# Performance work log

Measured on AMD Instinct MI355X. Metric: run time of the kernel, lower is better.

## Reference

```python
import jax, jax.numpy as jnp
import numpy as np

C = 128          # hidden_channels
N = 100000       # num nodes
E = 500000       # num edges
BN_EPS = 1e-5    # BatchNorm eps (training mode: batch statistics)


def _bn_relu(x, g, b):
    # BatchNorm1d (training mode, biased variance) followed by ReLU
    mu = x.mean(axis=0)
    var = x.var(axis=0)
    return jax.nn.relu(g * (x - mu) * jax.lax.rsqrt(var + BN_EPS) + b)


def setup_inputs() -> dict:
    key = jax.random.key(0)
    ks = jax.random.split(key, 10)
    f = lambda k, s: jax.random.normal(k, s, dtype=jnp.float32) * 0.05
    return {
        "node_rep": f(ks[0], (N, C)),
        "edge_rep": f(ks[1], (E, C)),
        "endpoints": jax.random.randint(ks[2], (2, E), 0, N, dtype=jnp.int64)
            if jax.config.jax_enable_x64 else jax.random.randint(ks[2], (2, E), 0, N, dtype=jnp.int32),
        # lvl_mlp_1: Linear(2C -> C, no bias) + BN(C)
        "W_lvl1": f(ks[3], (2 * C, C)),
        "g_lvl1": jnp.ones((C,), jnp.float32), "b_lvl1": jnp.zeros((C,), jnp.float32),
        # lvl_mlp_2: Linear(C->2C) + BN(2C) + ReLU + Linear(2C->C) + BN(C) + ReLU
        "W_n1": f(ks[4], (C, 2 * C)),
        "g_n1": jnp.ones((2 * C,), jnp.float32), "b_n1": jnp.zeros((2 * C,), jnp.float32),
        "W_n2": f(ks[5], (2 * C, C)),
        "g_n2": jnp.ones((C,), jnp.float32), "b_n2": jnp.zeros((C,), jnp.float32),
        # lift_mlp: Linear(C->2C) + BN(2C) + ReLU + Linear(2C->C) + BN(C) + ReLU
        "W_e1": f(ks[6], (C, 2 * C)),
        "g_e1": jnp.ones((2 * C,), jnp.float32), "b_e1": jnp.zeros((2 * C,), jnp.float32),
        "W_e2": f(ks[7], (2 * C, C)),
        "g_e2": jnp.ones((C,), jnp.float32), "b_e2": jnp.zeros((C,), jnp.float32),
        "eps1": jnp.zeros((), jnp.float32),
        "eps2": jnp.zeros((), jnp.float32),
    }


def reference(node_rep, edge_rep, endpoints,
              W_lvl1, g_lvl1, b_lvl1,
              W_n1, g_n1, b_n1, W_n2, g_n2, b_n2,
              W_e1, g_e1, b_e1, W_e2, g_e2, b_e2,
              eps1, eps2):
    s, t = endpoints[0], endpoints[1]
    # transfer0_0 node->edge: each edge sums its two endpoint node features
    lift_aggr = node_rep[s] + node_rep[t]                       # [E, C]
    h = _bn_relu(jnp.concatenate([lift_aggr, edge_rep], -1) @ W_lvl1,
                 g_lvl1, b_lvl1)                                # [E, C]
    # reverse transfer edge->node: scatter-add to both endpoints
    lvl_aggr = jnp.zeros_like(node_rep).at[s].add(h).at[t].add(h)  # [N, C]
    node_in = (1.0 + eps1) * node_rep + lvl_aggr
    node_out = _bn_relu(_bn_relu(node_in @ W_n1, g_n1, b_n1) @ W_n2, g_n2, b_n2)
    edge_in = (1.0 + eps2) * edge_rep + lift_aggr
    edge_out = _bn_relu(_bn_relu(edge_in @ W_e1, g_e1, b_e1) @ W_e2, g_e2, b_e2)
    return (node_out, edge_out)
```

## Files before the change

kernel.cpp:

```cpp
#include <hip/hip_runtime.h>

#define NN 100000
#define NE 500000

typedef short v8s __attribute__((ext_vector_type(8)));
typedef float v4f __attribute__((ext_vector_type(4)));

__device__ __forceinline__ unsigned short f2bf(float f) {
    unsigned u = __float_as_uint(f);
    u += 0x7fffu + ((u >> 16) & 1u);
    return (unsigned short)(u >> 16);
}
__device__ __forceinline__ float bf2f(unsigned short h) {
    return __uint_as_float(((unsigned)h) << 16);
}
__device__ __forceinline__ unsigned pk2(float a, float b) {
    return (unsigned)f2bf(a) | ((unsigned)f2bf(b) << 16);
}
__device__ __forceinline__ float lo16(unsigned v) { return bf2f((unsigned short)(v & 0xffffu)); }
__device__ __forceinline__ float hi16(unsigned v) { return bf2f((unsigned short)(v >> 16)); }

__device__ __forceinline__ unsigned load2(const void* base, long row, int lane, int f) {
    if (f) return ((const unsigned*)base)[row * 64 + lane];
    const float2 v = ((const float2*)base)[row * 64 + lane];
    return pk2(v.x, v.y);
}

__global__ void detect_k(const unsigned short* __restrict__ edgeR, int* __restrict__ flag) {
    __shared__ int cnt;
    const int tid = threadIdx.x;
    if (tid == 0) cnt = 0;
    __syncthreads();
    const float v = fabsf(bf2f(edgeR[2 * tid]));
    const int sane = (v > 1e-5f && v < 100.f) ? 1 : 0;
    atomicAdd(&cnt, sane);
    __syncthreads();
    if (tid == 0) *flag = (cnt >= 128) ? 1 : 0;
}

__global__ __launch_bounds__(256) void hist_k(const int* __restrict__ ep, int* __restrict__ deg) {
    const int i = blockIdx.x * 256 + threadIdx.x;
    if (i < 2 * NE) atomicAdd(&deg[ep[i]], 1);
}

__global__ __launch_bounds__(1024) void scan_k(int* __restrict__ degcur, int* __restrict__ rowptr) {
    __shared__ int sd[1024];
    const int t = threadIdx.x;
    const int base = t * 98;
    int sum = 0;
    for (int i = 0; i < 98; ++i) {
        const int idx = base + i;
        if (idx < NN) sum += degcur[idx];
    }
    sd[t] = sum;
    __syncthreads();
    for (int off = 1; off < 1024; off <<= 1) {
        const int v = (t >= off) ? sd[t - off] : 0;
        __syncthreads();
        sd[t] += v;
        __syncthreads();
    }
    int run = sd[t] - sum;
    for (int i = 0; i < 98; ++i) {
        const int idx = base + i;
        if (idx < NN) {
            const int d = degcur[idx];
            rowptr[idx] = run;
            degcur[idx] = run;
            run += d;
        }
    }
    if (t == 0) rowptr[NN] = 2 * NE;
}

__global__ __launch_bounds__(256) void fill_k(const int* __restrict__ ep,
                                              int* __restrict__ cursor, int* __restrict__ csr) {
    const int i = blockIdx.x * 256 + threadIdx.x;
    if (i >= 2 * NE) return;
    const int n = ep[i];
    const int pos = atomicAdd(&cursor[n], 1);
    csr[pos] = (i < NE) ? i : (i - NE);
}

__global__ __launch_bounds__(256) void pack_weights(
    const void* __restrict__ W1, const void* __restrict__ Wn1,
    const void* __restrict__ Wn2, const void* __restrict__ We1,
    const void* __restrict__ We2, unsigned short* __restrict__ wpk,
    const int* __restrict__ flag)
{
    const int i = blockIdx.x * 256 + threadIdx.x;
    if (i >= 163840) return;
    const void* W; int Nn; int li = i;
    if (i < 32768)       { W = W1;  Nn = 128; }
    else if (i < 65536)  { W = Wn1; Nn = 256; li -= 32768; }
    else if (i < 98304)  { W = Wn2; Nn = 128; li -= 65536; }
    else if (i < 131072) { W = We1; Nn = 256; li -= 98304; }
    else                 { W = We2; Nn = 128; li -= 131072; }
    const int ntn = Nn >> 4;
    const int j = li & 7, l = (li >> 3) & 63, tile = li >> 9;
    const int ct = tile % ntn, kt = tile / ntn;
    const int k = kt * 32 + (l >> 4) * 8 + j;
    const int n = ct * 16 + (l & 15);
    const int idx = k * Nn + n;
    wpk[i] = (*flag) ? ((const unsigned short*)W)[idx]
                     : f2bf(((const float*)W)[idx]);
}

__global__ __launch_bounds__(256, 5) void kernel_A(
    const void* __restrict__ node, const void* __restrict__ edge,
    const int* __restrict__ ep,
    const unsigned short* __restrict__ wpk1, const unsigned short* __restrict__ wpkE1,
    unsigned short* __restrict__ y1, unsigned short* __restrict__ edge_in,
    float* __restrict__ stats, const void* __restrict__ eps2p, const int* __restrict__ flag)
{
    __shared__ unsigned short X[64 * 256];
    const int tid = threadIdx.x, wid = tid >> 6, lane = tid & 63;
    const int mrow = lane & 15, quad = lane >> 4;
    const int li = lane & 31, hb = lane >> 5;
    const int e0 = blockIdx.x * 64;
    const int e0w = e0 + wid * 16;
    const int bin = blockIdx.x & 31;
    const int f = *flag;

    const int ei = e0w + mrow;
    int sv = 0, tv = 0;
    if (ei < NE) { sv = ep[ei]; tv = ep[NE + ei]; }

    #pragma unroll
    for (int j = 0; j < 8; ++j) {
        const int eA = e0w + 2 * j + hb;
        const int s = __shfl(sv, 2 * j + hb);
        const int t = __shfl(tv, 2 * j + hb);
        uint2 lp = {0u, 0u}, ee = {0u, 0u};
        if (eA < NE) {
            if (f) {
                const uint2 a = ((const uint2*)node)[s * 32 + li];
                const uint2 b = ((const uint2*)node)[t * 32 + li];
                ee = ((const uint2*)edge)[(size_t)eA * 32 + li];
                lp.x = pk2(lo16(a.x) + lo16(b.x), hi16(a.x) + hi16(b.x));
                lp.y = pk2(lo16(a.y) + lo16(b.y), hi16(a.y) + hi16(b.y));
            } else {
                const float4 a = ((const float4*)node)[s * 32 + li];
                const float4 b = ((const float4*)node)[t * 32 + li];
                const float4 ev = ((const float4*)edge)[(size_t)eA * 32 + li];
                lp.x = pk2(a.x + b.x, a.y + b.y);
                lp.y = pk2(a.z + b.z, a.w + b.w);
                ee.x = pk2(ev.x, ev.y);
                ee.y = pk2(ev.z, ev.w);
            }
        }
        const int r = wid * 16 + 2 * j + hb;
        const int swz = (r & 7) << 3;
        *(uint2*)&X[r * 256 + ((li * 4) ^ swz)] = lp;
        *(uint2*)&X[r * 256 + ((128 + li * 4) ^ swz)] = ee;
    }
    __syncthreads();

    {
        v4f acc[4][2];
        #pragma unroll
        for (int rb = 0; rb < 4; ++rb)
            #pragma unroll
            for (int c = 0; c < 2; ++c)
                acc[rb][c] = (v4f){0.f, 0.f, 0.f, 0.f};
        const int ct0 = wid * 2;
        #pragma unroll
        for (int kt = 0; kt < 8; ++kt) {
            v8s a[4];
            #pragma unroll
            for (int rb = 0; rb < 4; ++rb) {
                const int r = rb * 16 + mrow;
                a[rb] = *(const v8s*)&X[r * 256 + ((kt * 32 + quad * 8) ^ ((r & 7) << 3))];
            }
            #pragma unroll
            for (int c = 0; c < 2; ++c) {
                const v8s b = ((const v8s*)wpk1)[(kt * 8 + ct0 + c) * 64 + lane];
                #pragma unroll
                for (int rb = 0; rb < 4; ++rb)
                    acc[rb][c] = __builtin_amdgcn_mfma_f32_16x16x32_bf16(a[rb], b, acc[rb][c], 0, 0, 0);
            }
        }
        #pragma unroll
        for (int c = 0; c < 2; ++c) {
            const int col = (ct0 + c) * 16 + mrow;
            float sy = 0.f, sq = 0.f;
            #pragma unroll
            for (int rb = 0; rb < 4; ++rb) {
                #pragma unroll
                for (int r4 = 0; r4 < 4; ++r4) {
                    const float v = acc[rb][c][r4];
                    const int e = e0 + rb * 16 + quad * 4 + r4;
                    if (e < NE) y1[(size_t)e * 128 + col] = f2bf(v);
                    sy += v; sq += v * v;
                }
            }
            sy += __shfl_xor(sy, 16); sy += __shfl_xor(sy, 32);
            sq += __shfl_xor(sq, 16); sq += __shfl_xor(sq, 32);
            if (quad == 0) {
                atomicAdd(&stats[bin * 1792 + col], sy);
                atomicAdd(&stats[bin * 1792 + 128 + col], sq);
            }
        }
    }
    __syncthreads();

    const float e2 = 1.f + (f ? bf2f(((const unsigned short*)eps2p)[0])
                              : ((const float*)eps2p)[0]);
    #pragma unroll
    for (int rr = 0; rr < 16; ++rr) {
        const int r = wid * 16 + rr;
        const int swz = (r & 7) << 3;
        const unsigned lp = *(const unsigned*)&X[r * 256 + ((2 * lane) ^ swz)];
        const unsigned ee = *(const unsigned*)&X[r * 256 + ((128 + 2 * lane) ^ swz)];
        const unsigned o = pk2(fmaf(e2, lo16(ee), lo16(lp)), fmaf(e2, hi16(ee), hi16(lp)));
        *(unsigned*)&X[r * 256 + ((2 * lane) ^ swz)] = o;
        const int e = e0 + r;
        if (e < NE) ((unsigned*)edge_in)[(size_t)e * 64 + lane] = o;
    }
    __syncthreads();

    {
        v4f acc[4][4];
        #pragma unroll
        for (int rb = 0; rb < 4; ++rb)
            #pragma unroll
            for (int c = 0; c < 4; ++c)
                acc[rb][c] = (v4f){0.f, 0.f, 0.f, 0.f};
        const int ct0 = wid * 4;
        #pragma unroll
        for (int kt = 0; kt < 4; ++kt) {
            v8s a[4];
            #pragma unroll
            for (int rb = 0; rb < 4; ++rb) {
                const int r = rb * 16 + mrow;
                a[rb] = *(const v8s*)&X[r * 256 + ((kt * 32 + quad * 8) ^ ((r & 7) << 3))];
            }
            #pragma unroll
            for (int c = 0; c < 4; ++c) {
                const v8s b = ((const v8s*)wpkE1)[(kt * 16 + ct0 + c) * 64 + lane];
                #pragma unroll
                for (int rb = 0; rb < 4; ++rb)
                    acc[rb][c] = __builtin_amdgcn_mfma_f32_16x16x32_bf16(a[rb], b, acc[rb][c], 0, 0, 0);
            }
        }
        #pragma unroll
        for (int c = 0; c < 4; ++c) {
            const int col = (ct0 + c) * 16 + mrow;
            float sy = 0.f, sq = 0.f;
            #pragma unroll
            for (int rb = 0; rb < 4; ++rb) {
                #pragma unroll
                for (int r4 = 0; r4 < 4; ++r4) {
                    const float v = acc[rb][c][r4];
                    sy += v; sq += v * v;
                }
            }
            sy += __shfl_xor(sy, 16); sy += __shfl_xor(sy, 32);
            sq += __shfl_xor(sq, 16); sq += __shfl_xor(sq, 32);
            if (quad == 0) {
                atomicAdd(&stats[bin * 1792 + 256 + col], sy);
                atomicAdd(&stats[bin * 1792 + 512 + col], sq);
            }
        }
    }
}

__global__ void finalize_k(const float* __restrict__ stats, float* __restrict__ ab,
                           const void* __restrict__ g, const void* __restrict__ bb,
                           const int sOff, const int qOff, const int aOff, const int bOff,
                           const int n, const float invc, const int* __restrict__ flag)
{
    const int c = threadIdx.x;
    if (c >= n) return;
    float S = 0.f, Q = 0.f;
    for (int b = 0; b < 32; ++b) { S += stats[b * 1792 + sOff + c]; Q += stats[b * 1792 + qOff + c]; }
    const float mu = S * invc;
    const float var = Q * invc - mu * mu;
    const float gv = (*flag) ? bf2f(((const unsigned short*)g)[c]) : ((const float*)g)[c];
    const float bv = (*flag) ? bf2f(((const unsigned short*)bb)[c]) : ((const float*)bb)[c];
    const float a = gv * rsqrtf(var + 1e-5f);
    ab[aOff + c] = a;
    ab[bOff + c] = bv - a * mu;
}

__global__ __launch_bounds__(256, 5) void gemm_node1(
    const void* __restrict__ node, const unsigned short* __restrict__ y1,
    const int* __restrict__ rowptr, const int* __restrict__ csr,
    const unsigned short* __restrict__ wpk, unsigned short* __restrict__ node_in,
    float* __restrict__ sS, float* __restrict__ sQ,
    const void* __restrict__ eps1p, const float* __restrict__ ab,
    const int* __restrict__ flag)
{
    __shared__ unsigned short X[64 * 128];
    const int tid = threadIdx.x, wid = tid >> 6, lane = tid & 63;
    const int mrow = lane & 15, quad = lane >> 4;
    const long r0 = (long)blockIdx.x * 64;
    const int bin = blockIdx.x & 31;
    const int f = *flag;
    const float ea = 1.f + (f ? bf2f(((const unsigned short*)eps1p)[0])
                              : ((const float*)eps1p)[0]);
    const int c0 = 2 * lane;
    const float a0 = ab[c0], a1 = ab[c0 + 1];
    const float b0 = ab[128 + c0], b1 = ab[128 + c0 + 1];

    for (int rr = 0; rr < 16; ++rr) {
        const int r = wid * 16 + rr;
        const long gr = r0 + r;
        unsigned o = 0;
        if (gr < NN) {
            float s0 = 0.f, s1 = 0.f;
            const int beg = rowptr[gr], end = rowptr[gr + 1];
            for (int i = beg; i < end; ++i) {
                const int e = csr[i];
                const unsigned v = ((const unsigned*)y1)[(size_t)e * 64 + lane];
                s0 += fmaxf(fmaf(a0, lo16(v), b0), 0.f);
                s1 += fmaxf(fmaf(a1, hi16(v), b1), 0.f);
            }
            const unsigned nr = load2(node, gr, lane, f);
            o = pk2(fmaf(ea, lo16(nr), s0), fmaf(ea, hi16(nr), s1));
        }
        *(unsigned*)&X[r * 128 + ((2 * lane) ^ ((r & 7) << 3))] = o;
        if (gr < NN) ((unsigned*)node_in)[gr * 64 + lane] = o;
    }
    __syncthreads();

    v4f acc[4][4];
    #pragma unroll
    for (int rb = 0; rb < 4; ++rb)
        #pragma unroll
        for (int c = 0; c < 4; ++c)
            acc[rb][c] = (v4f){0.f, 0.f, 0.f, 0.f};
    const int ct0 = wid * 4;
    #pragma unroll
    for (int kt = 0; kt < 4; ++kt) {
        v8s a[4];
        #pragma unroll
        for (int rb = 0; rb < 4; ++rb) {
            const int r = rb * 16 + mrow;
            a[rb] = *(const v8s*)&X[r * 128 + ((kt * 32 + quad * 8) ^ ((r & 7) << 3))];
        }
        #pragma unroll
        for (int c = 0; c < 4; ++c) {
            const v8s b = ((const v8s*)wpk)[(kt * 16 + ct0 + c) * 64 + lane];
            #pragma unroll
            for (int rb = 0; rb < 4; ++rb)
                acc[rb][c] = __builtin_amdgcn_mfma_f32_16x16x32_bf16(a[rb], b, acc[rb][c], 0, 0, 0);
        }
    }
    #pragma unroll
    for (int c = 0; c < 4; ++c) {
        const int col = (ct0 + c) * 16 + mrow;
        float sy = 0.f, sq = 0.f;
        #pragma unroll
        for (int rb = 0; rb < 4; ++rb) {
            #pragma unroll
            for (int r4 = 0; r4 < 4; ++r4) {
                const float v = acc[rb][c][r4];
                sy += v; sq += v * v;
            }
        }
        sy += __shfl_xor(sy, 16); sy += __shfl_xor(sy, 32);
        sq += __shfl_xor(sq, 16); sq += __shfl_xor(sq, 32);
        if (quad == 0) {
            atomicAdd(&sS[bin * 1792 + col], sy);
            atomicAdd(&sQ[bin * 1792 + col], sq);
        }
    }
}

__global__ __launch_bounds__(256, 5) void fused2_k(
    const unsigned short* __restrict__ in, const float* __restrict__ aab,
    const float* __restrict__ bab, const unsigned short* __restrict__ wpkA,
    const unsigned short* __restrict__ wpkB, unsigned short* __restrict__ out,
    float* __restrict__ sS, float* __restrict__ sQ, const long rows)
{
    __shared__ unsigned short X[64 * 256];
    const int tid = threadIdx.x, wid = tid >> 6, lane = tid & 63;
    const int mrow = lane & 15, quad = lane >> 4;
    const long r0 = (long)blockIdx.x * 64;
    const int bin = blockIdx.x & 31;

    #pragma unroll
    for (int i = 0; i < 4; ++i) {
        const int r = wid * 16 + i * 4 + quad;
        const long gr = r0 + r;
        v8s v = (v8s){0, 0, 0, 0, 0, 0, 0, 0};
        if (gr < rows) v = *(const v8s*)(in + gr * 128 + mrow * 8);
        *(v8s*)&X[r * 256 + ((mrow * 8) ^ ((r & 7) << 3))] = v;
    }
    __syncthreads();

    v4f acc[4][4];
    #pragma unroll
    for (int rb = 0; rb < 4; ++rb)
        #pragma unroll
        for (int c = 0; c < 4; ++c)
            acc[rb][c] = (v4f){0.f, 0.f, 0.f, 0.f};
    const int ct0 = wid * 4;
    #pragma unroll
    for (int kt = 0; kt < 4; ++kt) {
        v8s a[4];
        #pragma unroll
        for (int rb = 0; rb < 4; ++rb) {
            const int r = rb * 16 + mrow;
            a[rb] = *(const v8s*)&X[r * 256 + ((kt * 32 + quad * 8) ^ ((r & 7) << 3))];
        }
        #pragma unroll
        for (int c = 0; c < 4; ++c) {
            const v8s b = ((const v8s*)wpkA)[(kt * 16 + ct0 + c) * 64 + lane];
            #pragma unroll
            for (int rb = 0; rb < 4; ++rb)
                acc[rb][c] = __builtin_amdgcn_mfma_f32_16x16x32_bf16(a[rb], b, acc[rb][c], 0, 0, 0);
        }
    }
    __syncthreads();

    #pragma unroll
    for (int c = 0; c < 4; ++c) {
        const int col = (ct0 + c) * 16 + mrow;
        const float av = aab[col], bv = bab[col];
        #pragma unroll
        for (int rb = 0; rb < 4; ++rb)
            #pragma unroll
            for (int r4 = 0; r4 < 4; ++r4) {
                const int r = rb * 16 + quad * 4 + r4;
                const float h = (r0 + r < rows) ? fmaxf(fmaf(av, acc[rb][c][r4], bv), 0.f) : 0.f;
                X[r * 256 + (col ^ ((r & 7) << 3))] = f2bf(h);
            }
    }
    __syncthreads();

    v4f acc2[4][2];
    #pragma unroll
    for (int rb = 0; rb < 4; ++rb)
        #pragma unroll
        for (int c = 0; c < 2; ++c)
            acc2[rb][c] = (v4f){0.f, 0.f, 0.f, 0.f};
    const int ct2 = wid * 2;
    #pragma unroll
    for (int kt = 0; kt < 8; ++kt) {
        v8s a[4];
        #pragma unroll
        for (int rb = 0; rb < 4; ++rb) {
            const int r = rb * 16 + mrow;
            a[rb] = *(const v8s*)&X[r * 256 + ((kt * 32 + quad * 8) ^ ((r & 7) << 3))];
        }
        #pragma unroll
        for (int c = 0; c < 2; ++c) {
            const v8s b = ((const v8s*)wpkB)[(kt * 8 + ct2 + c) * 64 + lane];
            #pragma unroll
            for (int rb = 0; rb < 4; ++rb)
                acc2[rb][c] = __builtin_amdgcn_mfma_f32_16x16x32_bf16(a[rb], b, acc2[rb][c], 0, 0, 0);
        }
    }
    #pragma unroll
    for (int c = 0; c < 2; ++c) {
        const int col = (ct2 + c) * 16 + mrow;
        float sy = 0.f, sq = 0.f;
        #pragma unroll
        for (int rb = 0; rb < 4; ++rb) {
            #pragma unroll
            for (int r4 = 0; r4 < 4; ++r4) {
                const float v = acc2[rb][c][r4];
                const long gr = r0 + rb * 16 + quad * 4 + r4;
                if (gr < rows) out[gr * 128 + col] = f2bf(v);
                sy += v; sq += v * v;
            }
        }
        sy += __shfl_xor(sy, 16); sy += __shfl_xor(sy, 32);
        sq += __shfl_xor(sq, 16); sq += __shfl_xor(sq, 32);
        if (quad == 0) {
            atomicAdd(&sS[bin * 1792 + col], sy);
            atomicAdd(&sQ[bin * 1792 + col], sq);
        }
    }
}

__global__ __launch_bounds__(256) void final_k(
    const unsigned short* __restrict__ z2, const unsigned short* __restrict__ w2,
    const float* __restrict__ ab, void* __restrict__ out, const int* __restrict__ flag)
{
    const long p = (long)blockIdx.x * 256 + threadIdx.x;
    const long npn = (long)NN * 32;
    const long tot = npn + (long)NE * 32;
    if (p >= tot) return;
    long el, oe; const unsigned short* src; int abA, abB;
    if (p < npn) { el = p * 4; oe = el; src = z2; abA = 1536; abB = 1664; }
    else { el = (p - npn) * 4; oe = (long)NN * 128 + el; src = w2; abA = 1280; abB = 1408; }
    const int col = (int)(el & 127);
    const uint2 v = *(const uint2*)(src + el);
    const float o0 = fmaxf(fmaf(ab[abA + col],     lo16(v.x), ab[abB + col]),     0.f);
    const float o1 = fmaxf(fmaf(ab[abA + col + 1], hi16(v.x), ab[abB + col + 1]), 0.f);
    const float o2 = fmaxf(fmaf(ab[abA + col + 2], lo16(v.y), ab[abB + col + 2]), 0.f);
    const float o3 = fmaxf(fmaf(ab[abA + col + 3], hi16(v.y), ab[abB + col + 3]), 0.f);
    if (*flag) {
        uint2 r; r.x = pk2(o0, o1); r.y = pk2(o2, o3);
        *(uint2*)((unsigned short*)out + oe) = r;
    } else {
        float4 f; f.x = o0; f.y = o1; f.z = o2; f.w = o3;
        *(float4*)((float*)out + oe) = f;
    }
}

extern "C" void kernel_launch(void* const* d_in, const int* in_sizes, int n_in,
                              void* d_out, int out_size, void* d_ws, size_t ws_size,
                              hipStream_t stream)
{
    (void)in_sizes; (void)n_in; (void)out_size; (void)ws_size;
    const unsigned short* edgeR = (const unsigned short*)d_in[1];
    const int* ep = (const int*)d_in[2];

    char* ws = (char*)d_ws;
    unsigned short* wpk = (unsigned short*)ws;
    float* stats   = (float*)(ws + 327680);
    float* ab      = (float*)(ws + 557056);
    int*   flag    = (int*)(ws + 564224);
    int*   rowptr  = (int*)(ws + 564480);
    int*   cursor  = (int*)(ws + 964608);
    int*   csr     = (int*)(ws + 1364736);
    unsigned short* y1      = (unsigned short*)(ws + 5364736);
    unsigned short* edge_in = (unsigned short*)(ws + 133364736);
    unsigned short* w2      = (unsigned short*)(ws + 261364736);
    unsigned short* node_in = (unsigned short*)(ws + 389364736);
    unsigned short* z2      = (unsigned short*)(ws + 414964736);

    const unsigned short* wpk1  = wpk;
    const unsigned short* wpkN1 = wpk + 32768;
    const unsigned short* wpkN2 = wpk + 65536;
    const unsigned short* wpkE1 = wpk + 98304;
    const unsigned short* wpkE2 = wpk + 131072;

    detect_k<<<1, 256, 0, stream>>>(edgeR, flag);
    hipMemsetAsync(stats, 0, 229376, stream);
    hipMemsetAsync(cursor, 0, 400000, stream);

    hist_k<<<3907, 256, 0, stream>>>(ep, cursor);
    scan_k<<<1, 1024, 0, stream>>>(cursor, rowptr);
    fill_k<<<3907, 256, 0, stream>>>(ep, cursor, csr);

    pack_weights<<<640, 256, 0, stream>>>(d_in[3], d_in[6], d_in[9], d_in[12], d_in[15], wpk, flag);

    kernel_A<<<7813, 256, 0, stream>>>(d_in[0], d_in[1], ep, wpk1, wpkE1, y1, edge_in, stats, d_in[19], flag);
    finalize_k<<<1, 128, 0, stream>>>(stats, ab, d_in[4], d_in[5], 0, 128, 0, 128, 128, 1.f / NE, flag);
    finalize_k<<<1, 256, 0, stream>>>(stats, ab, d_in[13], d_in[14], 256, 512, 256, 512, 256, 1.f / NE, flag);

    gemm_node1<<<1563, 256, 0, stream>>>(d_in[0], y1, rowptr, csr, wpkN1, node_in,
                                         stats + 768, stats + 1024, d_in[18], ab, flag);
    finalize_k<<<1, 256, 0, stream>>>(stats, ab, d_in[7], d_in[8], 768, 1024, 768, 1024, 256, 1.f / NN, flag);

    fused2_k<<<1563, 256, 0, stream>>>(node_in, ab + 768, ab + 1024, wpkN1, wpkN2, z2,
                                       stats + 1536, stats + 1664, (long)NN);
    finalize_k<<<1, 128, 0, stream>>>(stats, ab, d_in[10], d_in[11], 1536, 1664, 1536, 1664, 128, 1.f / NN, flag);

    fused2_k<<<7813, 256, 0, stream>>>(edge_in, ab + 256, ab + 512, wpkE1, wpkE2, w2,
                                       stats + 1280, stats + 1408, (long)NE);
    finalize_k<<<1, 128, 0, stream>>>(stats, ab, d_in[16], d_in[17], 1280, 1408, 1280, 1408, 128, 1.f / NE, flag);

    final_k<<<75000, 256, 0, stream>>>(z2, w2, ab, d_out, flag);
}
```

Measured before the change: 1.840 ms.

## Use nontemporal loads/stores, stage fused2 output through LDS, widen final_k vectors

Streaming global loads and stores in the edge/node kernels are switched to nontemporal builtins so single-use data bypasses cache retention. fused2_k's output is staged through shared memory and written as coalesced 16-byte row stores instead of scattered 2-byte stores. final_k now processes eight bf16 elements per thread with 16-byte accesses and half the grid. The LDS staging adds an extra barrier and shared-memory traffic, and the nontemporal hints could hurt if y1 is re-read later from cache.

New measurement: 1.769 ms. -3.9%, faster.

```diff
diff --git a/kernel.cpp b/kernel.cpp
--- a/kernel.cpp
+++ b/kernel.cpp
@@ -5,6 +5,9 @@
 
 typedef short v8s __attribute__((ext_vector_type(8)));
 typedef float v4f __attribute__((ext_vector_type(4)));
+typedef unsigned u32x2 __attribute__((ext_vector_type(2)));
+typedef unsigned u32x4 __attribute__((ext_vector_type(4)));
+typedef float f32x4 __attribute__((ext_vector_type(4)));
 
 __device__ __forceinline__ unsigned short f2bf(float f) {
     unsigned u = __float_as_uint(f);
@@ -131,18 +134,18 @@
         const int eA = e0w + 2 * j + hb;
         const int s = __shfl(sv, 2 * j + hb);
         const int t = __shfl(tv, 2 * j + hb);
-        uint2 lp = {0u, 0u}, ee = {0u, 0u};
+        u32x2 lp = {0u, 0u}, ee = {0u, 0u};
         if (eA < NE) {
             if (f) {
-                const uint2 a = ((const uint2*)node)[s * 32 + li];
-                const uint2 b = ((const uint2*)node)[t * 32 + li];
-                ee = ((const uint2*)edge)[(size_t)eA * 32 + li];
+                const u32x2 a = *(const u32x2*)((const unsigned*)node + (size_t)s * 64 + li * 2);
+                const u32x2 b = *(const u32x2*)((const unsigned*)node + (size_t)t * 64 + li * 2);
+                ee = __builtin_nontemporal_load((const u32x2*)((const unsigned*)edge + (size_t)eA * 64 + li * 2));
                 lp.x = pk2(lo16(a.x) + lo16(b.x), hi16(a.x) + hi16(b.x));
                 lp.y = pk2(lo16(a.y) + lo16(b.y), hi16(a.y) + hi16(b.y));
             } else {
-                const float4 a = ((const float4*)node)[s * 32 + li];
-                const float4 b = ((const float4*)node)[t * 32 + li];
-                const float4 ev = ((const float4*)edge)[(size_t)eA * 32 + li];
+                const f32x4 a = *(const f32x4*)((const float*)node + (size_t)s * 128 + li * 4);
+                const f32x4 b = *(const f32x4*)((const float*)node + (size_t)t * 128 + li * 4);
+                const f32x4 ev = __builtin_nontemporal_load((const f32x4*)((const float*)edge + (size_t)eA * 128 + li * 4));
                 lp.x = pk2(a.x + b.x, a.y + b.y);
                 lp.y = pk2(a.z + b.z, a.w + b.w);
                 ee.x = pk2(ev.x, ev.y);
@@ -151,8 +154,8 @@
         }
         const int r = wid * 16 + 2 * j + hb;
         const int swz = (r & 7) << 3;
-        *(uint2*)&X[r * 256 + ((li * 4) ^ swz)] = lp;
-        *(uint2*)&X[r * 256 + ((128 + li * 4) ^ swz)] = ee;
+        *(u32x2*)&X[r * 256 + ((li * 4) ^ swz)] = lp;
+        *(u32x2*)&X[r * 256 + ((128 + li * 4) ^ swz)] = ee;
     }
     __syncthreads();
 
@@ -190,7 +193,7 @@
                 for (int r4 = 0; r4 < 4; ++r4) {
                     const float v = acc[rb][c][r4];
                     const int e = e0 + rb * 16 + quad * 4 + r4;
-                    if (e < NE) y1[(size_t)e * 128 + col] = f2bf(v);
+                    if (e < NE) __builtin_nontemporal_store(f2bf(v), &y1[(size_t)e * 128 + col]);
                     sy += v; sq += v * v;
                 }
             }
@@ -215,7 +218,7 @@
         const unsigned o = pk2(fmaf(e2, lo16(ee), lo16(lp)), fmaf(e2, hi16(ee), hi16(lp)));
         *(unsigned*)&X[r * 256 + ((2 * lane) ^ swz)] = o;
         const int e = e0 + r;
-        if (e < NE) ((unsigned*)edge_in)[(size_t)e * 64 + lane] = o;
+        if (e < NE) __builtin_nontemporal_store(o, &((unsigned*)edge_in)[(size_t)e * 64 + lane]);
     }
     __syncthreads();
 
@@ -320,7 +323,7 @@
             o = pk2(fmaf(ea, lo16(nr), s0), fmaf(ea, hi16(nr), s1));
         }
         *(unsigned*)&X[r * 128 + ((2 * lane) ^ ((r & 7) << 3))] = o;
-        if (gr < NN) ((unsigned*)node_in)[gr * 64 + lane] = o;
+        if (gr < NN) __builtin_nontemporal_store(o, &((unsigned*)node_in)[gr * 64 + lane]);
     }
     __syncthreads();
 
@@ -385,7 +388,7 @@
         const int r = wid * 16 + i * 4 + quad;
         const long gr = r0 + r;
         v8s v = (v8s){0, 0, 0, 0, 0, 0, 0, 0};
-        if (gr < rows) v = *(const v8s*)(in + gr * 128 + mrow * 8);
+        if (gr < rows) v = __builtin_nontemporal_load((const v8s*)(in + gr * 128 + mrow * 8));
         *(v8s*)&X[r * 256 + ((mrow * 8) ^ ((r & 7) << 3))] = v;
     }
     __syncthreads();
@@ -462,8 +465,6 @@
             #pragma unroll
             for (int r4 = 0; r4 < 4; ++r4) {
                 const float v = acc2[rb][c][r4];
-                const long gr = r0 + rb * 16 + quad * 4 + r4;
-                if (gr < rows) out[gr * 128 + col] = f2bf(v);
                 sy += v; sq += v * v;
             }
         }
@@ -474,6 +475,30 @@
             atomicAdd(&sQ[bin * 1792 + col], sq);
         }
     }
+    __syncthreads();
+
+    #pragma unroll
+    for (int c = 0; c < 2; ++c) {
+        const int col = (ct2 + c) * 16 + mrow;
+        #pragma unroll
+        for (int rb = 0; rb < 4; ++rb)
+            #pragma unroll
+            for (int r4 = 0; r4 < 4; ++r4) {
+                const int r = rb * 16 + quad * 4 + r4;
+                X[r * 256 + (col ^ ((r & 7) << 3))] = f2bf(acc2[rb][c][r4]);
+            }
+    }
+    __syncthreads();
+
+    #pragma unroll
+    for (int i = 0; i < 4; ++i) {
+        const int r = wid * 16 + i * 4 + quad;
+        const long gr = r0 + r;
+        if (gr < rows) {
+            const u32x4 v = *(const u32x4*)&X[r * 256 + ((mrow * 8) ^ ((r & 7) << 3))];
+            __builtin_nontemporal_store(v, (u32x4*)(out + gr * 128 + mrow * 8));
+        }
+    }
 }
 
 __global__ __launch_bounds__(256) void final_k(
@@ -481,24 +506,32 @@
     const float* __restrict__ ab, void* __restrict__ out, const int* __restrict__ flag)
 {
     const long p = (long)blockIdx.x * 256 + threadIdx.x;
-    const long npn = (long)NN * 32;
-    const long tot = npn + (long)NE * 32;
+    const long npn = (long)NN * 16;
+    const long tot = npn + (long)NE * 16;
     if (p >= tot) return;
     long el, oe; const unsigned short* src; int abA, abB;
-    if (p < npn) { el = p * 4; oe = el; src = z2; abA = 1536; abB = 1664; }
-    else { el = (p - npn) * 4; oe = (long)NN * 128 + el; src = w2; abA = 1280; abB = 1408; }
+    if (p < npn) { el = p * 8; oe = el; src = z2; abA = 1536; abB = 1664; }
+    else { el = (p - npn) * 8; oe = (long)NN * 128 + el; src = w2; abA = 1280; abB = 1408; }
     const int col = (int)(el & 127);
-    const uint2 v = *(const uint2*)(src + el);
-    const float o0 = fmaxf(fmaf(ab[abA + col],     lo16(v.x), ab[abB + col]),     0.f);
-    const float o1 = fmaxf(fmaf(ab[abA + col + 1], hi16(v.x), ab[abB + col + 1]), 0.f);
-    const float o2 = fmaxf(fmaf(ab[abA + col + 2], lo16(v.y), ab[abB + col + 2]), 0.f);
-    const float o3 = fmaxf(fmaf(ab[abA + col + 3], hi16(v.y), ab[abB + col + 3]), 0.f);
+    const u32x4 v = __builtin_nontemporal_load((const u32x4*)(src + el));
+    float o[8];
+    #pragma unroll
+    for (int i = 0; i < 4; ++i) {
+        o[2 * i]     = fmaxf(fmaf(ab[abA + col + 2 * i],     lo16(v[i]), ab[abB + col + 2 * i]),     0.f);
+        o[2 * i + 1] = fmaxf(fmaf(ab[abA + col + 2 * i + 1], hi16(v[i]), ab[abB + col + 2 * i + 1]), 0.f);
+    }
     if (*flag) {
-        uint2 r; r.x = pk2(o0, o1); r.y = pk2(o2, o3);
-        *(uint2*)((unsigned short*)out + oe) = r;
+        u32x4 r;
+        #pragma unroll
+        for (int i = 0; i < 4; ++i) r[i] = pk2(o[2 * i], o[2 * i + 1]);
+        __builtin_nontemporal_store(r, (u32x4*)((unsigned short*)out + oe));
     } else {
-        float4 f; f.x = o0; f.y = o1; f.z = o2; f.w = o3;
-        *(float4*)((float*)out + oe) = f;
+        f32x4 r0, r1;
+        r0.x = o[0]; r0.y = o[1]; r0.z = o[2]; r0.w = o[3];
+        r1.x = o[4]; r1.y = o[5]; r1.z = o[6]; r1.w = o[7];
+        float* op = (float*)out + oe;
+        __builtin_nontemporal_store(r0, (f32x4*)op);
+        __builtin_nontemporal_store(r1, (f32x4*)(op + 4));
     }
 }
 
@@ -556,5 +589,5 @@
                                        stats + 1280, stats + 1408, (long)NE);
     finalize_k<<<1, 128, 0, stream>>>(stats, ab, d_in[16], d_in[17], 1280, 1408, 1280, 1408, 128, 1.f / NE, flag);
 
-    final_k<<<75000, 256, 0, stream>>>(z2, w2, ab, d_out, flag);
-}
+    final_k<<<37500, 256, 0, stream>>>(z2, w2, ab, d_out, flag);
+}
```
